# Performance work log

Measured on AMD Instinct MI355X. Metric: run time of the kernel, lower is better.

Reference implementation:

```python
import jax, jax.numpy as jnp
import numpy as np

B, M, C, IMG, P, D, L, H, DFF, NC = 16, 4, 3, 224, 16, 768, 12, 12, 3072, 1000
G = IMG // P
S = G * G + 1
HD = D // H
EPS = 1e-6
SCALE = HD ** -0.5


def setup_inputs() -> dict:
    key = jax.random.key(0)
    ks = jax.random.split(key, 12)
    w = lambda k, shape: (jax.random.normal(k, shape) * 0.02).astype(jnp.float32)
    return {
        'x': jax.random.normal(ks[0], (B, C, IMG, IMG), jnp.float32),
        'x_tangent': jax.random.normal(ks[1], (B, M, C, IMG, IMG), jnp.float32),
        'patch_w': w(ks[2], (D, C * P * P)), 'patch_b': jnp.zeros((D,), jnp.float32),
        'cls_token': w(ks[3], (1, 1, D)), 'pos_embed': w(ks[4], (1, S, D)),
        'ln1_g': jnp.ones((L, D), jnp.float32), 'ln1_b': jnp.zeros((L, D), jnp.float32),
        'qkv_w': w(ks[5], (L, 3 * D, D)), 'qkv_b': jnp.zeros((L, 3 * D), jnp.float32),
        'proj_w': w(ks[6], (L, D, D)), 'proj_b': jnp.zeros((L, D), jnp.float32),
        'ln2_g': jnp.ones((L, D), jnp.float32), 'ln2_b': jnp.zeros((L, D), jnp.float32),
        'fc1_w': w(ks[7], (L, DFF, D)), 'fc1_b': jnp.zeros((L, DFF), jnp.float32),
        'fc2_w': w(ks[8], (L, D, DFF)), 'fc2_b': jnp.zeros((L, D), jnp.float32),
        'normf_g': jnp.ones((D,), jnp.float32), 'normf_b': jnp.zeros((D,), jnp.float32),
        'head_w': w(ks[9], (NC, D)), 'head_b': jnp.zeros((NC,), jnp.float32),
    }


def _patchify(img):
    # [b,C,IMG,IMG] -> [b, G*G, C*P*P], matching Conv2d(patch) weight layout (c, ph, pw)
    b = img.shape[0]
    p = img.reshape(b, C, G, P, G, P).transpose(0, 2, 4, 1, 3, 5)
    return p.reshape(b, G * G, C * P * P)


def _ln_jvp(x, t, g, b):
    # x: [B,S,D], t: [B,M,S,D]; params constant w.r.t. tangent directions
    mu = x.mean(-1, keepdims=True)
    xc = x - mu
    inv = jax.lax.rsqrt((xc * xc).mean(-1, keepdims=True) + EPS)
    xh = xc * inv
    y = xh * g + b
    xh_b, inv_b = xh[:, None], inv[:, None]
    ty = g * inv_b * (t - t.mean(-1, keepdims=True) - xh_b * (xh_b * t).mean(-1, keepdims=True))
    return y, ty


def _gelu_jvp(x, t):
    # exact (erf) GELU and its derivative; x: [B,S,F], t: [B,M,S,F]
    cdf = 0.5 * (1.0 + jax.lax.erf(x * 0.7071067811865476))
    pdf = jnp.exp(-0.5 * x * x) * 0.3989422804014327
    return x * cdf, t * (cdf + x * pdf)[:, None]


def _softmax_jvp(s, ts):
    # s: [B,H,S,S], ts: [B,M,H,S,S]
    a = jax.nn.softmax(s, axis=-1)
    a_b = a[:, None]
    ta = a_b * (ts - (a_b * ts).sum(-1, keepdims=True))
    return a, ta


def reference(x, x_tangent, patch_w, patch_b, cls_token, pos_embed,
              ln1_g, ln1_b, qkv_w, qkv_b, proj_w, proj_b, ln2_g, ln2_b,
              fc1_w, fc1_b, fc2_w, fc2_b, normf_g, normf_b, head_w, head_b):
    # patch embed (primal + tangent; bias/pos/cls are constants -> zero tangent)
    h = _patchify(x) @ patch_w.T + patch_b                                  # [B,N,D]
    th = (_patchify(x_tangent.reshape(B * M, C, IMG, IMG)) @ patch_w.T).reshape(B, M, G * G, D)
    cls = jnp.broadcast_to(cls_token, (B, 1, D))
    h = jnp.concatenate([cls, h], axis=1) + pos_embed                       # [B,S,D]
    th = jnp.concatenate([jnp.zeros((B, M, 1, D), th.dtype), th], axis=2)   # [B,M,S,D]

    for l in range(L):
        # --- attention (manual JVP, matching the torch einsum path) ---
        y, ty = _ln_jvp(h, th, ln1_g[l], ln1_b[l])
        qkv = y @ qkv_w[l].T + qkv_b[l]
        tqkv = ty @ qkv_w[l].T
        q, k, v = jnp.split(qkv, 3, axis=-1)
        tq, tk, tv = jnp.split(tqkv, 3, axis=-1)
        q = q.reshape(B, S, H, HD); k = k.reshape(B, S, H, HD); v = v.reshape(B, S, H, HD)
        tq = tq.reshape(B, M, S, H, HD); tk = tk.reshape(B, M, S, H, HD); tv = tv.reshape(B, M, S, H, HD)
        s = jnp.einsum('bqhd,bkhd->bhqk', q, k) * SCALE
        ts = (jnp.einsum('bmqhd,bkhd->bmhqk', tq, k)
              + jnp.einsum('bqhd,bmkhd->bmhqk', q, tk)) * SCALE
        a, ta = _softmax_jvp(s, ts)
        o = jnp.einsum('bhqk,bkhd->bqhd', a, v).reshape(B, S, D)
        to = (jnp.einsum('bmhqk,bkhd->bmqhd', ta, v)
              + jnp.einsum('bhqk,bmkhd->bmqhd', a, tv)).reshape(B, M, S, D)
        h = h + o @ proj_w[l].T + proj_b[l]
        th = th + to @ proj_w[l].T
        # --- mlp ---
        y, ty = _ln_jvp(h, th, ln2_g[l], ln2_b[l])
        y = y @ fc1_w[l].T + fc1_b[l]
        ty = ty @ fc1_w[l].T
        y, ty = _gelu_jvp(y, ty)
        h = h + y @ fc2_w[l].T + fc2_b[l]
        th = th + ty @ fc2_w[l].T

    y, ty = _ln_jvp(h, th, normf_g, normf_b)
    logits = y[:, 0] @ head_w.T + head_b            # token pooling
    tlogits = ty[:, :, 0] @ head_w.T                 # [B,M,NC]
    return logits, tlogits
```

## Files before the change

kernel.cpp:

```cpp
#include <hip/hip_runtime.h>
#include <hip/hip_bf16.h>

#define DEVI __device__ __forceinline__

typedef short  bf16x8 __attribute__((ext_vector_type(8)));
typedef float  f32x4  __attribute__((ext_vector_type(4)));
typedef float  f32x4v __attribute__((ext_vector_type(4)));

static constexpr int BB   = 16;
static constexpr int MM   = 4;
static constexpr int CC   = 3;
static constexpr int IMG  = 224;
static constexpr int PPP  = 16;
static constexpr int DD   = 768;
static constexpr int LL   = 12;
static constexpr int HH   = 12;
static constexpr int DFF  = 3072;
static constexpr int NCLS = 1000;
static constexpr int GG   = 14;
static constexpr int SS   = 197;
static constexpr int HD   = 64;
static constexpr int BT   = BB*SS;
static constexpr int BMT  = BB*MM*SS;
static constexpr int RT   = BT+BMT;
static constexpr int RP   = 15872;
static constexpr int SP   = 208;
static constexpr int QLD  = 3*DD;
static constexpr int PRP  = BB*GG*GG;
static constexpr int PRT  = (BB+BB*MM)*GG*GG;
static constexpr float EPSV  = 1e-6f;
static constexpr float SCALE = 0.125f;

static constexpr int NQW  = QLD*DD;
static constexpr int NPW  = DD*DD;
static constexpr int NF1W = DFF*DD;
static constexpr int NF2W = DD*DFF;
static constexpr int WTOT = NQW+NPW+NF1W+NF2W;

DEVI unsigned short f2bf(float x){
  union { float f; unsigned u; } v; v.f = x;
  unsigned r = v.u + 0x7fffu + ((v.u>>16)&1u);
  return (unsigned short)(r>>16);
}
DEVI float bf2f(unsigned short x){
  union { unsigned u; float f; } v; v.u = ((unsigned)x)<<16;
  return v.f;
}
DEVI f32x4 mfma16(bf16x8 a, bf16x8 b, f32x4 c){
  return __builtin_amdgcn_mfma_f32_16x16x32_bf16(a,b,c,0,0,0);
}
typedef const void __attribute__((address_space(1)))* gas1;
typedef void __attribute__((address_space(3)))* las3;


DEVI bf16x8 cvt8(const float* src){
  float4 a = *(const float4*)src;
  float4 b = *(const float4*)(src+4);
  bf16x8 o;
  o[0]=(short)f2bf(a.x); o[1]=(short)f2bf(a.y); o[2]=(short)f2bf(a.z); o[3]=(short)f2bf(a.w);
  o[4]=(short)f2bf(b.x); o[5]=(short)f2bf(b.y); o[6]=(short)f2bf(b.z); o[7]=(short)f2bf(b.w);
  return o;
}

__global__ __launch_bounds__(256) void f2bf8_kernel(const float* __restrict__ in,
    unsigned short* __restrict__ out, size_t n8){
  size_t i = (size_t)blockIdx.x*256 + threadIdx.x;
  if (i < n8) *(bf16x8*)(out + i*8) = cvt8(in + i*8);
}

__global__ __launch_bounds__(256) void conv_all_v(const float* __restrict__ qkvw,
    const float* __restrict__ projw, const float* __restrict__ f1w,
    const float* __restrict__ f2w, unsigned short* __restrict__ wl){
  int l = blockIdx.y;
  size_t i = ((size_t)blockIdx.x*256 + threadIdx.x)*8;
  const float* src;
  if (i < NQW)                src = qkvw + (size_t)l*NQW + i;
  else if (i < NQW+NPW)       src = projw + (size_t)l*NPW + (i-NQW);
  else if (i < NQW+NPW+NF1W)  src = f1w + (size_t)l*NF1W + (i-NQW-NPW);
  else                        src = f2w + (size_t)l*NF2W + (i-NQW-NPW-NF1W);
  *(bf16x8*)(wl + (size_t)l*WTOT + i) = cvt8(src);
}

__global__ __launch_bounds__(256) void conv_layer_v(const float* __restrict__ qkvw,
    const float* __restrict__ projw, const float* __restrict__ f1w,
    const float* __restrict__ f2w, unsigned short* __restrict__ wl){
  size_t i = ((size_t)blockIdx.x*256 + threadIdx.x)*8;
  const float* src;
  if (i < NQW)                src = qkvw + i;
  else if (i < NQW+NPW)       src = projw + (i-NQW);
  else if (i < NQW+NPW+NF1W)  src = f1w + (i-NQW-NPW);
  else                        src = f2w + (i-NQW-NPW-NF1W);
  *(bf16x8*)(wl + i) = cvt8(src);
}

__global__ __launch_bounds__(256) void init_h(float* __restrict__ hh,
    const float* __restrict__ cls, const float* __restrict__ pos,
    const float* __restrict__ patch_b){
  size_t i = (size_t)blockIdx.x*256 + threadIdx.x;
  int r = (int)(i/DD), c = (int)(i%DD);
  float v = 0.f;
  if (r < BT){
    int s_ = r % SS;
    v = pos[(size_t)s_*DD + c] + (s_==0 ? cls[c] : patch_b[c]);
  }
  hh[i] = v;
}

__global__ __launch_bounds__(256) void patchify_k(const float* __restrict__ x,
    const float* __restrict__ xt, unsigned short* __restrict__ pat){
  size_t i = (size_t)blockIdx.x*256 + threadIdx.x;
  int r = (int)(i/DD), kk = (int)(i%DD);
  int c = kk>>8, rem = kk&255, py = rem>>4, px = rem&15;
  const float* src;
  if (r < PRP){
    int b_ = r/(GG*GG), p = r%(GG*GG);
    src = x + (((size_t)b_*CC + c)*IMG + (size_t)(p/GG)*PPP + py)*IMG + (p%GG)*PPP + px;
  } else {
    int rr = r-PRP; int bm = rr/(GG*GG), p = rr%(GG*GG);
    src = xt + (((size_t)bm*CC + c)*IMG + (size_t)(p/GG)*PPP + py)*IMG + (p%GG)*PPP + px;
  }
  pat[i] = f2bf(*src);
}


DEVI void blockSum4(float&a,float&b,float&c,float&d,float* red){
  #pragma unroll
  for (int off=32; off; off>>=1){
    a += __shfl_xor(a,off,64); b += __shfl_xor(b,off,64);
    c += __shfl_xor(c,off,64); d += __shfl_xor(d,off,64);
  }
  int w = threadIdx.x>>6;
  if ((threadIdx.x&63)==0){ red[w]=a; red[4+w]=b; red[8+w]=c; red[12+w]=d; }
  __syncthreads();
  a = red[0]+red[1]+red[2]+red[3];
  b = red[4]+red[5]+red[6]+red[7];
  c = red[8]+red[9]+red[10]+red[11];
  d = red[12]+red[13]+red[14]+red[15];
  __syncthreads();
}

__global__ __launch_bounds__(256) void ln_group(const float* __restrict__ hh,
    const float* __restrict__ g, const float* __restrict__ bb,
    unsigned short* __restrict__ ybf){
  __shared__ float red[4][10];
  int r = blockIdx.x;
  int b_ = r/SS, s_ = r%SS;
  int t = threadIdx.x;
  const float* xx = hh + (size_t)r*DD;
  float x0=xx[t], x1=xx[t+256], x2=xx[t+512];
  size_t trow[4];
  float tv[4][3];
  #pragma unroll
  for (int m=0;m<4;m++){
    trow[m] = (size_t)BT + ((size_t)(b_*MM+m))*SS + s_;
    const float* tt = hh + trow[m]*DD;
    tv[m][0]=tt[t]; tv[m][1]=tt[t+256]; tv[m][2]=tt[t+512];
  }
  float s[10];
  s[0]=x0+x1+x2; s[1]=x0*x0+x1*x1+x2*x2;
  #pragma unroll
  for (int m=0;m<4;m++){
    s[2+2*m]=tv[m][0]+tv[m][1]+tv[m][2];
    s[3+2*m]=x0*tv[m][0]+x1*tv[m][1]+x2*tv[m][2];
  }
  #pragma unroll
  for (int k=0;k<10;k++){
    float v = s[k];
    #pragma unroll
    for (int off=32; off; off>>=1) v += __shfl_xor(v, off, 64);
    s[k] = v;
  }
  int w = t>>6;
  if ((t&63)==0){
    #pragma unroll
    for (int k=0;k<10;k++) red[w][k]=s[k];
  }
  __syncthreads();
  #pragma unroll
  for (int k=0;k<10;k++) s[k] = red[0][k]+red[1][k]+red[2][k]+red[3][k];
  float mu  = s[0]*(1.f/DD);
  float inv = rsqrtf(s[1]*(1.f/DD) - mu*mu + EPSV);
  float g0=g[t], g1=g[t+256], g2=g[t+512];
  float h0=(x0-mu)*inv, h1=(x1-mu)*inv, h2=(x2-mu)*inv;
  {
    unsigned short* y = ybf + (size_t)r*DD;
    y[t]     = f2bf(h0*g0 + bb[t]);
    y[t+256] = f2bf(h1*g1 + bb[t+256]);
    y[t+512] = f2bf(h2*g2 + bb[t+512]);
  }
  #pragma unroll
  for (int m=0;m<4;m++){
    float tmean = s[2+2*m]*(1.f/DD);
    float dot   = inv*(s[3+2*m]*(1.f/DD) - mu*tmean);
    unsigned short* y = ybf + trow[m]*DD;
    y[t]     = f2bf(g0*inv*(tv[m][0] - tmean - h0*dot));
    y[t+256] = f2bf(g1*inv*(tv[m][1] - tmean - h1*dot));
    y[t+512] = f2bf(g2*inv*(tv[m][2] - tmean - h2*dot));
  }
}

__global__ __launch_bounds__(256) void ln_head(const float* __restrict__ hh,
    const float* __restrict__ g, const float* __restrict__ bb,
    unsigned short* __restrict__ ybf){
  __shared__ float red[16];
  int ri = blockIdx.x;
  int t = threadIdx.x;
  if (ri < BB){
    size_t row = (size_t)ri*SS;
    const float* x = hh + row*DD;
    float x0=x[t], x1=x[t+256], x2=x[t+512];
    float s1=x0+x1+x2, s2=x0*x0+x1*x1+x2*x2, s3=0.f, s4=0.f;
    blockSum4(s1,s2,s3,s4,red);
    float mu  = s1*(1.f/DD);
    float inv = rsqrtf(s2*(1.f/DD) - mu*mu + EPSV);
    unsigned short* y = ybf + row*DD;
    y[t]     = f2bf((x0-mu)*inv*g[t]     + bb[t]);
    y[t+256] = f2bf((x1-mu)*inv*g[t+256] + bb[t+256]);
    y[t+512] = f2bf((x2-mu)*inv*g[t+512] + bb[t+512]);
  } else {
    int t2 = ri - BB;
    size_t row = (size_t)BT + (size_t)t2*SS;
    size_t prow = (size_t)(t2/MM)*SS;
    const float* tt = hh + row*DD;
    const float* xx = hh + prow*DD;
    float t0=tt[t], t1=tt[t+256], t2v=tt[t+512];
    float x0=xx[t], x1=xx[t+256], x2=xx[t+512];
    float s1=x0+x1+x2, s2=x0*x0+x1*x1+x2*x2;
    float s3=t0+t1+t2v, s4=x0*t0+x1*t1+x2*t2v;
    blockSum4(s1,s2,s3,s4,red);
    float mu  = s1*(1.f/DD);
    float inv = rsqrtf(s2*(1.f/DD) - mu*mu + EPSV);
    float tmean = s3*(1.f/DD);
    float dot   = inv*(s4*(1.f/DD) - mu*tmean);
    unsigned short* y = ybf + row*DD;
    y[t]     = f2bf(g[t]    *inv*(t0  - tmean - (x0-mu)*inv*dot));
    y[t+256] = f2bf(g[t+256]*inv*(t1  - tmean - (x1-mu)*inv*dot));
    y[t+512] = f2bf(g[t+512]*inv*(t2v - tmean - (x2-mu)*inv*dot));
  }
}


template<int MODE>
__global__ __launch_bounds__(256,2) void gemm_bt(
    const unsigned short* __restrict__ A,
    const unsigned short* __restrict__ Aalt, int asplit, int lda,
    const unsigned short* __restrict__ W, int K, int N, int Mrows,
    float* __restrict__ outf, unsigned short* __restrict__ outb, int ldc,
    const float* __restrict__ bias, int bias_limit)
{
  __shared__ __attribute__((aligned(16))) unsigned short As[128*64];
  __shared__ __attribute__((aligned(16))) unsigned short Bs[128*64];
  const int tid = threadIdx.x;
  const int wave = tid>>6, lane = tid&63;
  const int tM = blockIdx.y, tN = blockIdx.x;
  f32x4 acc[4][4];
  f32x4 zf = {0.f,0.f,0.f,0.f};
  #pragma unroll
  for (int m=0;m<4;m++)
    #pragma unroll
    for (int n=0;n<4;n++) acc[m][n] = zf;
  const int wm = wave>>1, wn = wave&1;
  const int lrow = lane&15, lk8 = (lane>>4)<<3;
  const int srow = tid>>3;
  const int scol = (tid&7)<<3;
  const size_t arow0 = (size_t)tM*128;
  const size_t brow0 = (size_t)tN*128;

  for (int k0=0; k0<K; k0+=64){
    #pragma unroll
    for (int i=0;i<4;i++){
      int row = (int)arow0 + srow + i*32;
      const unsigned short* abase = (row < asplit) ? Aalt : A;
      const unsigned short* ga = abase + (size_t)row*lda + (k0+scol);
      __builtin_amdgcn_global_load_lds((gas1)ga, (las3)(As + i*2048 + wave*512), 16, 0, 0);
      const unsigned short* gb = W + (brow0+srow+i*32)*(size_t)K + (k0+scol);
      __builtin_amdgcn_global_load_lds((gas1)gb, (las3)(Bs + i*2048 + wave*512), 16, 0, 0);
    }
    __syncthreads();
    #pragma unroll
    for (int kk=0; kk<64; kk+=32){
      bf16x8 af[4], bw[4];
      #pragma unroll
      for (int m=0;m<4;m++) af[m] = *(const bf16x8*)(As + (wm*64+m*16+lrow)*64 + kk+lk8);
      #pragma unroll
      for (int n=0;n<4;n++) bw[n] = *(const bf16x8*)(Bs + (wn*64+n*16+lrow)*64 + kk+lk8);
      #pragma unroll
      for (int m=0;m<4;m++)
        #pragma unroll
        for (int n=0;n<4;n++)
          acc[m][n] = mfma16(af[m], bw[n], acc[m][n]);
    }
    __syncthreads();
  }

  const int colbase = tN*128 + wn*64 + lrow;
  const int rowbase = tM*128 + wm*64 + ((lane>>4)<<2);
  #pragma unroll
  for (int n=0;n<4;n++){
    int col = colbase + n*16;
    #pragma unroll
    for (int m=0;m<4;m++){
      #pragma unroll
      for (int i=0;i<4;i++){
        int r = rowbase + m*16 + i;
        float v = acc[m][n][i];
        if (MODE==0){
          if (r < bias_limit) v += bias[col];
          outb[(size_t)r*ldc + col] = f2bf(v);
        } else if (MODE==1){
          if (r < Mrows){
            if (r < bias_limit) v += bias[col];
            outf[(size_t)r*ldc + col] += v;
          }
        } else {
          if (r < PRT){
            int orow;
            if (r < PRP) orow = (r/196)*197 + 1 + r%196;
            else { int rr = r-PRP; orow = BT + (rr/196)*197 + 1 + rr%196; }
            outf[(size_t)orow*ldc + col] += v;
          }
        }
      }
    }
  }
}

__global__ __launch_bounds__(256) void transpose_v(const unsigned short* __restrict__ qkv,
    unsigned short* __restrict__ vT, unsigned short* __restrict__ tvT){
  __shared__ unsigned short tile[SP*65];
  int inst = blockIdx.x;
  size_t rowbase; unsigned short* dst; int h;
  if (inst < BB*HH){ int b_=inst/HH; h=inst%HH; rowbase=(size_t)b_*SS; dst = vT + (size_t)inst*HD*SP; }
  else { int i2=inst-BB*HH; int bm=i2/HH; h=i2%HH; rowbase=(size_t)BT+(size_t)bm*SS; dst = tvT + (size_t)i2*HD*SP; }
  int coff = 2*DD + h*HD;
  for (int i=threadIdx.x; i<SP*HD; i+=256){
    int k = i>>6, d = i&63;
    unsigned short v = (k<SS) ? qkv[(rowbase+k)*QLD + coff + d] : (unsigned short)0;
    tile[k*65+d] = v;
  }
  __syncthreads();
  for (int i=threadIdx.x; i<HD*SP; i+=256){
    int d = i/SP, k = i%SP;
    dst[(size_t)d*SP + k] = tile[k*65+d];
  }
}

__global__ __launch_bounds__(256) void attn_s1(const unsigned short* __restrict__ qkv,
                                               unsigned short* __restrict__ abf){
  int qt = blockIdx.x, inst = blockIdx.y;
  int wave = threadIdx.x>>6, lane = threadIdx.x&63;
  int lrow = lane&15, lk = (lane>>4)<<3;
  int q0 = qt*64 + wave*16;
  f32x4 acc[13];
  f32x4 zf = {0.f,0.f,0.f,0.f};
  #pragma unroll
  for (int n=0;n<13;n++) acc[n]=zf;
  int h = inst % HH, b_ = inst / HH;
  size_t prow = (size_t)b_*SS;
  const unsigned short* Ab = qkv + (prow + q0 + lrow)*QLD + h*HD + lk;
  const unsigned short* Bb = qkv + prow*QLD + DD + h*HD + lk;
  #pragma unroll
  for (int kk=0; kk<HD; kk+=32){
    bf16x8 av = *(const bf16x8*)(Ab + kk);
    #pragma unroll
    for (int n=0;n<13;n++){
      bf16x8 bv = *(const bf16x8*)(Bb + (size_t)(n*16+lrow)*QLD + kk);
      acc[n] = mfma16(av, bv, acc[n]);
    }
  }
  int grp = lane>>4;
  unsigned short* obase = abf + (size_t)inst*SP*SP;
  bool okc12 = (lrow < 5);
  #pragma unroll
  for (int i=0;i<4;i++){
    int qr = q0 + grp*4 + i;
    float val[13], e[13];
    float mv = -1e30f;
    #pragma unroll
    for (int n=0;n<13;n++){
      val[n] = acc[n][i]*SCALE;
      if (n<12 || okc12) mv = fmaxf(mv, val[n]);
    }
    #pragma unroll
    for (int off=8; off; off>>=1) mv = fmaxf(mv, __shfl_xor(mv, off, 64));
    float s = 0.f;
    #pragma unroll
    for (int n=0;n<13;n++){
      e[n] = (n<12 || okc12) ? __expf(val[n]-mv) : 0.f;
      s += e[n];
    }
    #pragma unroll
    for (int off=8; off; off>>=1) s += __shfl_xor(s, off, 64);
    float inv = 1.f/s;
    if (qr < SS){
      unsigned short* orow = obase + (size_t)qr*SP;
      #pragma unroll
      for (int n=0;n<13;n++) orow[n*16+lrow] = f2bf(e[n]*inv);
    }
  }
}

__global__ __launch_bounds__(256) void attn_s2(const unsigned short* __restrict__ qkv,
    const unsigned short* __restrict__ abf, unsigned short* __restrict__ tabf,
    int bmix0){
  int qt = blockIdx.x, il = blockIdx.y;
  int wave = threadIdx.x>>6, lane = threadIdx.x&63;
  int lrow = lane&15, lk = (lane>>4)<<3;
  int q0 = qt*64 + wave*16;
  f32x4 acc[13];
  f32x4 zf = {0.f,0.f,0.f,0.f};
  #pragma unroll
  for (int n=0;n<13;n++) acc[n]=zf;
  int h = il % HH;
  int bmix = bmix0 + il / HH;
  int b_ = bmix / MM;
  int bh = b_*HH + h;
  size_t prow = (size_t)b_*SS;
  size_t trow = (size_t)BT + (size_t)bmix*SS;
  #pragma unroll
  for (int p=0;p<2;p++){
    size_t ar = (p==0) ? trow : prow;
    size_t br = (p==1) ? trow : prow;
    const unsigned short* Ab = qkv + (ar + q0 + lrow)*QLD + h*HD + lk;
    const unsigned short* Bb = qkv + br*QLD + DD + h*HD + lk;
    #pragma unroll
    for (int kk=0; kk<HD; kk+=32){
      bf16x8 av = *(const bf16x8*)(Ab + kk);
      #pragma unroll
      for (int n=0;n<13;n++){
        bf16x8 bv = *(const bf16x8*)(Bb + (size_t)(n*16+lrow)*QLD + kk);
        acc[n] = mfma16(av, bv, acc[n]);
      }
    }
  }
  int grp = lane>>4;
  const unsigned short* abase = abf + (size_t)bh*SP*SP;
  unsigned short* tbase = tabf + (size_t)il*SP*SP;
  #pragma unroll
  for (int i=0;i<4;i++){
    int qr = q0 + grp*4 + i;
    int qc = (qr < SS) ? qr : (SS-1);
    const unsigned short* arow = abase + (size_t)qc*SP;
    float av[13], tv[13];
    float dot = 0.f;
    #pragma unroll
    for (int n=0;n<13;n++){
      tv[n] = acc[n][i]*SCALE;
      av[n] = bf2f(arow[n*16+lrow]);
      dot += av[n]*tv[n];
    }
    #pragma unroll
    for (int off=8; off; off>>=1) dot += __shfl_xor(dot, off, 64);
    if (qr < SS){
      unsigned short* trow_ = tbase + (size_t)qr*SP;
      #pragma unroll
      for (int n=0;n<13;n++) trow_[n*16+lrow] = f2bf(av[n]*(tv[n]-dot));
    }
  }
}

template<int NP>
__global__ __launch_bounds__(256) void attn_pv(
    const unsigned short* __restrict__ abf, const unsigned short* __restrict__ tabf,
    const unsigned short* __restrict__ vT,  const unsigned short* __restrict__ tvT,
    unsigned short* __restrict__ obf, int bmix0){
  int qt = blockIdx.x, il = blockIdx.y;
  int wave = threadIdx.x>>6, lane = threadIdx.x&63;
  int lrow = lane&15, lk = (lane>>4)<<3;
  int q0 = qt*64 + wave*16;
  int h = il % HH;
  int bmix = (NP==1) ? (il/HH) : (bmix0 + il/HH);
  int b_ = (NP==1) ? bmix : bmix/MM;
  int bh = b_*HH + h;
  f32x4 acc[4];
  f32x4 zf = {0.f,0.f,0.f,0.f};
  #pragma unroll
  for (int n=0;n<4;n++) acc[n]=zf;
  int arow = q0 + lrow; if (arow > SP-1) arow = SP-1;
  #pragma unroll
  for (int p=0;p<NP;p++){
    const unsigned short* Ab = (NP==2 && p==0) ? tabf + (size_t)il*SP*SP
                                               : abf + (size_t)bh*SP*SP;
    const unsigned short* Bb = (NP==2 && p==1) ? tvT + (size_t)(bmix*HH+h)*HD*SP
                                               : vT + (size_t)bh*HD*SP;
    #pragma unroll
    for (int ks=0; ks<6; ks++){
      int kb = ks*32 + lk;
      bf16x8 av = *(const bf16x8*)(Ab + (size_t)arow*SP + kb);
      #pragma unroll
      for (int n=0;n<4;n++){
        bf16x8 bv = *(const bf16x8*)(Bb + (size_t)(n*16+lrow)*SP + kb);
        acc[n] = mfma16(av, bv, acc[n]);
      }
    }
    {
      int kb = 192 + lk;
      const bf16x8 ZV = {0,0,0,0,0,0,0,0};
      bool ok = (lk < 16);
      bf16x8 av = ok ? *(const bf16x8*)(Ab + (size_t)arow*SP + kb) : ZV;
      #pragma unroll
      for (int n=0;n<4;n++){
        bf16x8 bv = ok ? *(const bf16x8*)(Bb + (size_t)(n*16+lrow)*SP + kb) : ZV;
        acc[n] = mfma16(av, bv, acc[n]);
      }
    }
  }
  size_t orow0 = (NP==1) ? (size_t)bmix*SS : (size_t)BT + (size_t)bmix*SS;
  int qr0 = q0 + ((lane>>4)<<2);
  #pragma unroll
  for (int n=0;n<4;n++){
    int cc = h*HD + n*16 + lrow;
    #pragma unroll
    for (int i=0;i<4;i++){
      int qr = qr0 + i;
      if (qr < SS) obf[(orow0+qr)*DD + cc] = f2bf(acc[n][i]);
    }
  }
}

__global__ __launch_bounds__(256) void gelu_group(unsigned short* __restrict__ fc1o,
                                                  unsigned short* __restrict__ pgbf){
  int r = blockIdx.x;
  int b_ = r/SS, s_ = r%SS;
  const bf16x8* pb = (const bf16x8*)(fc1o + (size_t)r*DFF);
  bf16x8* pg = (bf16x8*)(pgbf + (size_t)r*DFF);
  bf16x8* tb[4];
  #pragma unroll
  for (int m=0;m<4;m++)
    tb[m] = (bf16x8*)(fc1o + ((size_t)BT + (size_t)(b_*MM+m)*SS + s_)*DFF);
  for (int c = threadIdx.x; c < DFF/8; c += 256){
    bf16x8 xv = pb[c];
    float deriv[8];
    bf16x8 o;
    #pragma unroll
    for (int j=0;j<8;j++){
      float x = bf2f((unsigned short)xv[j]);
      float cdf = 0.5f*(1.f + erff(x*0.70710678118654752f));
      float pdf = __expf(-0.5f*x*x)*0.39894228040143267f;
      o[j] = (short)f2bf(x*cdf);
      deriv[j] = cdf + x*pdf;
    }
    pg[c] = o;
    #pragma unroll
    for (int m=0;m<4;m++){
      bf16x8 tv8 = tb[m][c];
      bf16x8 w;
      #pragma unroll
      for (int j=0;j<8;j++) w[j] = (short)f2bf(bf2f((unsigned short)tv8[j])*deriv[j]);
      tb[m][c] = w;
    }
  }
}

__global__ __launch_bounds__(256) void head_k(const unsigned short* __restrict__ ybf,
    const float* __restrict__ hw, const float* __restrict__ hb, float* __restrict__ out){
  __shared__ float ysh[DD];
  int ri = blockIdx.x;
  size_t yrow; float* o; bool wb;
  if (ri < BB){ yrow = (size_t)ri*SS; o = out + (size_t)ri*NCLS; wb = true; }
  else { int t2 = ri-BB; yrow = (size_t)BT + (size_t)t2*SS; o = out + (size_t)BB*NCLS + (size_t)t2*NCLS; wb = false; }
  for (int d=threadIdx.x; d<DD; d+=256) ysh[d] = bf2f(ybf[yrow*DD + d]);
  __syncthreads();
  for (int n=threadIdx.x; n<NCLS; n+=256){
    const float* wrow = hw + (size_t)n*DD;
    float acc = wb ? hb[n] : 0.f;
    for (int d=0; d<DD; d++) acc += ysh[d]*wrow[d];
    o[n] = acc;
  }
}

extern "C" void kernel_launch(void* const* d_in, const int* in_sizes, int n_in,
                              void* d_out, int out_size, void* d_ws, size_t ws_size,
                              hipStream_t stream)
{
  const float* x      = (const float*)d_in[0];
  const float* xt     = (const float*)d_in[1];
  const float* patch_w= (const float*)d_in[2];
  const float* patch_b= (const float*)d_in[3];
  const float* cls    = (const float*)d_in[4];
  const float* pos    = (const float*)d_in[5];
  const float* ln1_g  = (const float*)d_in[6];
  const float* ln1_b  = (const float*)d_in[7];
  const float* qkv_w  = (const float*)d_in[8];
  const float* qkv_b  = (const float*)d_in[9];
  const float* proj_w = (const float*)d_in[10];
  const float* proj_b = (const float*)d_in[11];
  const float* ln2_g  = (const float*)d_in[12];
  const float* ln2_b  = (const float*)d_in[13];
  const float* fc1_w  = (const float*)d_in[14];
  const float* fc1_b  = (const float*)d_in[15];
  const float* fc2_w  = (const float*)d_in[16];
  const float* fc2_b  = (const float*)d_in[17];
  const float* nf_g   = (const float*)d_in[18];
  const float* nf_b   = (const float*)d_in[19];
  const float* head_w = (const float*)d_in[20];
  const float* head_b = (const float*)d_in[21];
  float* out = (float*)d_out;

  char* ws = (char*)d_ws;
  size_t off = 0;
  auto alloc = [&](size_t bytes)->char*{
    char* p = ws + off;
    off = (off + bytes + 255) & ~(size_t)255;
    return p;
  };

  unsigned short *w_patch, *wl, *ybf, *qkvbf, *vT, *tvT, *abf, *tabf, *fc1o, *pgbf;
  float *hh;
  auto layout = [&](bool allw, int nbm)->size_t{
    off = 0;
    w_patch = (unsigned short*)alloc((size_t)DD*DD*2);
    wl      = (unsigned short*)alloc((size_t)WTOT*2*(allw?LL:1));
    hh      = (float*)alloc((size_t)RP*DD*4);
    ybf     = (unsigned short*)alloc((size_t)RP*DD*2);
    size_t slab0 = off;
    qkvbf = (unsigned short*)alloc((size_t)RP*QLD*2);
    vT    = (unsigned short*)alloc((size_t)BB*HH*HD*SP*2);
    tvT   = (unsigned short*)alloc((size_t)BB*MM*HH*HD*SP*2);
    abf   = (unsigned short*)alloc((size_t)BB*HH*SP*SP*2);
    tabf  = (unsigned short*)alloc((size_t)nbm*HH*SP*SP*2);
    size_t endA = off;
    off = slab0;
    fc1o = (unsigned short*)alloc((size_t)RP*DFF*2);
    pgbf = (unsigned short*)alloc((size_t)BT*DFF*2);
    size_t endB = off;
    return (endA > endB) ? endA : endB;
  };

  bool allw = true; int nbm = BB*MM;
  size_t need = layout(true, BB*MM);
  if (need > ws_size){ need = layout(true, BB*MM/4);  allw=true;  nbm=BB*MM/4; }
  if (need > ws_size){ need = layout(false, BB*MM);   allw=false; nbm=BB*MM;   }
  if (need > ws_size){ need = layout(false, BB*MM/4); allw=false; nbm=BB*MM/4; }
  if (need > ws_size){
    hipMemsetAsync(d_out, 0x7f, (size_t)out_size*4, stream);
    return;
  }
  int nch = (BB*MM)/nbm;

  dim3 blk(256);
  f2bf8_kernel<<<dim3((DD*DD/8+255)/256), blk, 0, stream>>>(patch_w, w_patch, (size_t)DD*DD/8);
  if (allw)
    conv_all_v<<<dim3(WTOT/8/256, LL), blk, 0, stream>>>(qkv_w, proj_w, fc1_w, fc2_w, wl);
  init_h<<<dim3((RP*DD)/256), blk, 0, stream>>>(hh, cls, pos, patch_b);
  patchify_k<<<dim3((PRT*DD)/256), blk, 0, stream>>>(x, xt, ybf);
  gemm_bt<2><<<dim3(DD/128, 123), blk, 0, stream>>>(ybf, nullptr, 0, DD, w_patch, DD, DD, PRT,
                                                    hh, nullptr, DD, nullptr, 0);

  for (int l=0; l<LL; l++){
    if (!allw)
      conv_layer_v<<<dim3(WTOT/8/256), blk, 0, stream>>>(qkv_w+(size_t)l*NQW, proj_w+(size_t)l*NPW,
                                                         fc1_w+(size_t)l*NF1W, fc2_w+(size_t)l*NF2W, wl);
    const unsigned short* w_qkv = wl + (allw ? (size_t)l*WTOT : 0);
    const unsigned short* w_proj= w_qkv + NQW;
    const unsigned short* w_fc1 = w_qkv + NQW + NPW;
    const unsigned short* w_fc2 = w_qkv + NQW + NPW + NF1W;

    ln_group<<<dim3(BT), blk, 0, stream>>>(hh, ln1_g+(size_t)l*DD, ln1_b+(size_t)l*DD, ybf);
    gemm_bt<0><<<dim3(QLD/128, RP/128), blk, 0, stream>>>(ybf, nullptr, 0, DD, w_qkv,
        DD, QLD, RT, nullptr, qkvbf, QLD, qkv_b+(size_t)l*QLD, BT);
    transpose_v<<<dim3(BB*HH + BB*MM*HH), blk, 0, stream>>>(qkvbf, vT, tvT);
    attn_s1<<<dim3(4, BB*HH), blk, 0, stream>>>(qkvbf, abf);
    attn_pv<1><<<dim3(4, BB*HH), blk, 0, stream>>>(abf, nullptr, vT, nullptr, ybf, 0);
    for (int c=0; c<nch; c++){
      attn_s2<<<dim3(4, nbm*HH), blk, 0, stream>>>(qkvbf, abf, tabf, c*nbm);
      attn_pv<2><<<dim3(4, nbm*HH), blk, 0, stream>>>(abf, tabf, vT, tvT, ybf, c*nbm);
    }
    gemm_bt<1><<<dim3(DD/128, RP/128), blk, 0, stream>>>(ybf, nullptr, 0, DD, w_proj,
        DD, DD, RT, hh, nullptr, DD, proj_b+(size_t)l*DD, BT);
    ln_group<<<dim3(BT), blk, 0, stream>>>(hh, ln2_g+(size_t)l*DD, ln2_b+(size_t)l*DD, ybf);
    gemm_bt<0><<<dim3(DFF/128, RP/128), blk, 0, stream>>>(ybf, nullptr, 0, DD, w_fc1,
        DD, DFF, RT, nullptr, fc1o, DFF, fc1_b+(size_t)l*DFF, BT);
    gelu_group<<<dim3(BT), blk, 0, stream>>>(fc1o, pgbf);
    gemm_bt<1><<<dim3(DD/128, RP/128), blk, 0, stream>>>(fc1o, pgbf, BT, DFF, w_fc2,
        DFF, DD, RT, hh, nullptr, DD, fc2_b+(size_t)l*DD, BT);
  }

  ln_head<<<dim3(BB + BB*MM), blk, 0, stream>>>(hh, nf_g, nf_b, ybf);
  head_k<<<dim3(BB + BB*MM), blk, 0, stream>>>(ybf, head_w, head_b, out);
}
```

Before: 7.969 ms.

## Fuse attention score/softmax with PV matmul via shared-memory probability tiles

Merges the softmax stage and the PV matmul into one kernel for both the primal and tangent attention paths. Probabilities and tangent probabilities are staged in LDS, so the tangent probability buffer (tabf) is no longer written to and re-read from global memory. Removing tabf also removes the chunked launch loop and its workspace fallback. The cost is 27–54 KB of LDS per block, which may lower occupancy, plus extra block-wide syncs.

```diff
diff --git a/kernel.cpp b/kernel.cpp
--- a/kernel.cpp
+++ b/kernel.cpp
@@ -5,7 +5,6 @@
 
 typedef short  bf16x8 __attribute__((ext_vector_type(8)));
 typedef float  f32x4  __attribute__((ext_vector_type(4)));
-typedef float  f32x4v __attribute__((ext_vector_type(4)));
 
 static constexpr int BB   = 16;
 static constexpr int MM   = 4;
@@ -25,6 +24,7 @@
 static constexpr int RT   = BT+BMT;
 static constexpr int RP   = 15872;
 static constexpr int SP   = 208;
+static constexpr int LDP  = 216;
 static constexpr int QLD  = 3*DD;
 static constexpr int PRP  = BB*GG*GG;
 static constexpr int PRT  = (BB+BB*MM)*GG*GG;
@@ -345,8 +345,10 @@
   }
 }
 
-__global__ __launch_bounds__(256) void attn_s1(const unsigned short* __restrict__ qkv,
-                                               unsigned short* __restrict__ abf){
+__global__ __launch_bounds__(256) void attn_s1_pv(const unsigned short* __restrict__ qkv,
+    unsigned short* __restrict__ abf, const unsigned short* __restrict__ vT,
+    unsigned short* __restrict__ obf){
+  __shared__ __attribute__((aligned(16))) unsigned short pa[64*LDP];
   int qt = blockIdx.x, inst = blockIdx.y;
   int wave = threadIdx.x>>6, lane = threadIdx.x&63;
   int lrow = lane&15, lk = (lane>>4)<<3;
@@ -392,29 +394,81 @@
     #pragma unroll
     for (int off=8; off; off>>=1) s += __shfl_xor(s, off, 64);
     float inv = 1.f/s;
-    if (qr < SS){
-      unsigned short* orow = obase + (size_t)qr*SP;
-      #pragma unroll
-      for (int n=0;n<13;n++) orow[n*16+lrow] = f2bf(e[n]*inv);
-    }
-  }
-}
-
-__global__ __launch_bounds__(256) void attn_s2(const unsigned short* __restrict__ qkv,
-    const unsigned short* __restrict__ abf, unsigned short* __restrict__ tabf,
-    int bmix0){
+    unsigned short* lrp = pa + (size_t)(wave*16 + grp*4 + i)*LDP;
+    unsigned short* orow = obase + (size_t)qr*SP;
+    #pragma unroll
+    for (int n=0;n<13;n++){
+      unsigned short pv_ = f2bf(e[n]*inv);
+      lrp[n*16+lrow] = pv_;
+      if (qr < SS) orow[n*16+lrow] = pv_;
+    }
+  }
+  __syncthreads();
+  f32x4 pacc[4];
+  #pragma unroll
+  for (int n=0;n<4;n++) pacc[n]=zf;
+  const unsigned short* Vb = vT + (size_t)inst*HD*SP;
+  const unsigned short* Arow = pa + (size_t)(wave*16 + lrow)*LDP;
+  #pragma unroll
+  for (int ks=0; ks<6; ks++){
+    int kb = ks*32 + lk;
+    bf16x8 av = *(const bf16x8*)(Arow + kb);
+    #pragma unroll
+    for (int n=0;n<4;n++){
+      bf16x8 bv = *(const bf16x8*)(Vb + (size_t)(n*16+lrow)*SP + kb);
+      pacc[n] = mfma16(av, bv, pacc[n]);
+    }
+  }
+  {
+    int kb = 192 + lk;
+    const bf16x8 ZV = {0,0,0,0,0,0,0,0};
+    bool ok = (lk < 16);
+    bf16x8 av = ok ? *(const bf16x8*)(Arow + kb) : ZV;
+    #pragma unroll
+    for (int n=0;n<4;n++){
+      bf16x8 bv = ok ? *(const bf16x8*)(Vb + (size_t)(n*16+lrow)*SP + kb) : ZV;
+      pacc[n] = mfma16(av, bv, pacc[n]);
+    }
+  }
+  size_t orow0 = (size_t)b_*SS;
+  int qr0 = q0 + (grp<<2);
+  #pragma unroll
+  for (int n=0;n<4;n++){
+    int cc = h*HD + n*16 + lrow;
+    #pragma unroll
+    for (int i=0;i<4;i++){
+      int qr = qr0 + i;
+      if (qr < SS) obf[(orow0+qr)*DD + cc] = f2bf(pacc[n][i]);
+    }
+  }
+}
+
+__global__ __launch_bounds__(256) void attn_s2_pv(const unsigned short* __restrict__ qkv,
+    const unsigned short* __restrict__ abf, const unsigned short* __restrict__ vT,
+    const unsigned short* __restrict__ tvT, unsigned short* __restrict__ obf){
+  __shared__ __attribute__((aligned(16))) unsigned short sa[64*LDP];
+  __shared__ __attribute__((aligned(16))) unsigned short ta[64*LDP];
   int qt = blockIdx.x, il = blockIdx.y;
   int wave = threadIdx.x>>6, lane = threadIdx.x&63;
   int lrow = lane&15, lk = (lane>>4)<<3;
   int q0 = qt*64 + wave*16;
+  int h = il % HH;
+  int bmix = il / HH;
+  int b_ = bmix / MM;
+  int bh = b_*HH + h;
+  {
+    const unsigned short* abase = abf + (size_t)bh*SP*SP;
+    int qb = qt*64;
+    for (int c = threadIdx.x; c < 64*26; c += 256){
+      int rl = c/26, c8 = (c%26)*8;
+      int qr = qb + rl; if (qr > SS-1) qr = SS-1;
+      *(bf16x8*)(sa + (size_t)rl*LDP + c8) = *(const bf16x8*)(abase + (size_t)qr*SP + c8);
+    }
+  }
   f32x4 acc[13];
   f32x4 zf = {0.f,0.f,0.f,0.f};
   #pragma unroll
   for (int n=0;n<13;n++) acc[n]=zf;
-  int h = il % HH;
-  int bmix = bmix0 + il / HH;
-  int b_ = bmix / MM;
-  int bh = b_*HH + h;
   size_t prow = (size_t)b_*SS;
   size_t trow = (size_t)BT + (size_t)bmix*SS;
   #pragma unroll
@@ -433,14 +487,12 @@
       }
     }
   }
+  __syncthreads();
   int grp = lane>>4;
-  const unsigned short* abase = abf + (size_t)bh*SP*SP;
-  unsigned short* tbase = tabf + (size_t)il*SP*SP;
   #pragma unroll
   for (int i=0;i<4;i++){
-    int qr = q0 + grp*4 + i;
-    int qc = (qr < SS) ? qr : (SS-1);
-    const unsigned short* arow = abase + (size_t)qc*SP;
+    int rl = wave*16 + grp*4 + i;
+    const unsigned short* arow = sa + (size_t)rl*LDP;
     float av[13], tv[13];
     float dot = 0.f;
     #pragma unroll
@@ -451,69 +503,50 @@
     }
     #pragma unroll
     for (int off=8; off; off>>=1) dot += __shfl_xor(dot, off, 64);
-    if (qr < SS){
-      unsigned short* trow_ = tbase + (size_t)qr*SP;
-      #pragma unroll
-      for (int n=0;n<13;n++) trow_[n*16+lrow] = f2bf(av[n]*(tv[n]-dot));
-    }
-  }
-}
-
-template<int NP>
-__global__ __launch_bounds__(256) void attn_pv(
-    const unsigned short* __restrict__ abf, const unsigned short* __restrict__ tabf,
-    const unsigned short* __restrict__ vT,  const unsigned short* __restrict__ tvT,
-    unsigned short* __restrict__ obf, int bmix0){
-  int qt = blockIdx.x, il = blockIdx.y;
-  int wave = threadIdx.x>>6, lane = threadIdx.x&63;
-  int lrow = lane&15, lk = (lane>>4)<<3;
-  int q0 = qt*64 + wave*16;
-  int h = il % HH;
-  int bmix = (NP==1) ? (il/HH) : (bmix0 + il/HH);
-  int b_ = (NP==1) ? bmix : bmix/MM;
-  int bh = b_*HH + h;
-  f32x4 acc[4];
-  f32x4 zf = {0.f,0.f,0.f,0.f};
-  #pragma unroll
-  for (int n=0;n<4;n++) acc[n]=zf;
-  int arow = q0 + lrow; if (arow > SP-1) arow = SP-1;
-  #pragma unroll
-  for (int p=0;p<NP;p++){
-    const unsigned short* Ab = (NP==2 && p==0) ? tabf + (size_t)il*SP*SP
-                                               : abf + (size_t)bh*SP*SP;
-    const unsigned short* Bb = (NP==2 && p==1) ? tvT + (size_t)(bmix*HH+h)*HD*SP
-                                               : vT + (size_t)bh*HD*SP;
+    unsigned short* trp = ta + (size_t)rl*LDP;
+    #pragma unroll
+    for (int n=0;n<13;n++) trp[n*16+lrow] = f2bf(av[n]*(tv[n]-dot));
+  }
+  __syncthreads();
+  f32x4 pacc[4];
+  #pragma unroll
+  for (int n=0;n<4;n++) pacc[n]=zf;
+  #pragma unroll
+  for (int p=0;p<2;p++){
+    const unsigned short* Arow = (p==0 ? ta : sa) + (size_t)(wave*16 + lrow)*LDP;
+    const unsigned short* Bb = (p==0) ? vT + (size_t)bh*HD*SP
+                                      : tvT + (size_t)il*HD*SP;
     #pragma unroll
     for (int ks=0; ks<6; ks++){
       int kb = ks*32 + lk;
-      bf16x8 av = *(const bf16x8*)(Ab + (size_t)arow*SP + kb);
+      bf16x8 av = *(const bf16x8*)(Arow + kb);
       #pragma unroll
       for (int n=0;n<4;n++){
         bf16x8 bv = *(const bf16x8*)(Bb + (size_t)(n*16+lrow)*SP + kb);
-        acc[n] = mfma16(av, bv, acc[n]);
+        pacc[n] = mfma16(av, bv, pacc[n]);
       }
     }
     {
       int kb = 192 + lk;
       const bf16x8 ZV = {0,0,0,0,0,0,0,0};
       bool ok = (lk < 16);
-      bf16x8 av = ok ? *(const bf16x8*)(Ab + (size_t)arow*SP + kb) : ZV;
+      bf16x8 av = ok ? *(const bf16x8*)(Arow + kb) : ZV;
       #pragma unroll
       for (int n=0;n<4;n++){
         bf16x8 bv = ok ? *(const bf16x8*)(Bb + (size_t)(n*16+lrow)*SP + kb) : ZV;
-        acc[n] = mfma16(av, bv, acc[n]);
+        pacc[n] = mfma16(av, bv, pacc[n]);
       }
     }
   }
-  size_t orow0 = (NP==1) ? (size_t)bmix*SS : (size_t)BT + (size_t)bmix*SS;
-  int qr0 = q0 + ((lane>>4)<<2);
+  size_t orow0 = (size_t)BT + (size_t)bmix*SS;
+  int qr0 = q0 + (grp<<2);
   #pragma unroll
   for (int n=0;n<4;n++){
     int cc = h*HD + n*16 + lrow;
     #pragma unroll
     for (int i=0;i<4;i++){
       int qr = qr0 + i;
-      if (qr < SS) obf[(orow0+qr)*DD + cc] = f2bf(acc[n][i]);
+      if (qr < SS) obf[(orow0+qr)*DD + cc] = f2bf(pacc[n][i]);
     }
   }
 }
@@ -605,9 +638,9 @@
     return p;
   };
 
-  unsigned short *w_patch, *wl, *ybf, *qkvbf, *vT, *tvT, *abf, *tabf, *fc1o, *pgbf;
+  unsigned short *w_patch, *wl, *ybf, *qkvbf, *vT, *tvT, *abf, *fc1o, *pgbf;
   float *hh;
-  auto layout = [&](bool allw, int nbm)->size_t{
+  auto layout = [&](bool allw)->size_t{
     off = 0;
     w_patch = (unsigned short*)alloc((size_t)DD*DD*2);
     wl      = (unsigned short*)alloc((size_t)WTOT*2*(allw?LL:1));
@@ -618,7 +651,6 @@
     vT    = (unsigned short*)alloc((size_t)BB*HH*HD*SP*2);
     tvT   = (unsigned short*)alloc((size_t)BB*MM*HH*HD*SP*2);
     abf   = (unsigned short*)alloc((size_t)BB*HH*SP*SP*2);
-    tabf  = (unsigned short*)alloc((size_t)nbm*HH*SP*SP*2);
     size_t endA = off;
     off = slab0;
     fc1o = (unsigned short*)alloc((size_t)RP*DFF*2);
@@ -627,16 +659,13 @@
     return (endA > endB) ? endA : endB;
   };
 
-  bool allw = true; int nbm = BB*MM;
-  size_t need = layout(true, BB*MM);
-  if (need > ws_size){ need = layout(true, BB*MM/4);  allw=true;  nbm=BB*MM/4; }
-  if (need > ws_size){ need = layout(false, BB*MM);   allw=false; nbm=BB*MM;   }
-  if (need > ws_size){ need = layout(false, BB*MM/4); allw=false; nbm=BB*MM/4; }
+  bool allw = true;
+  size_t need = layout(true);
+  if (need > ws_size){ need = layout(false); allw = false; }
   if (need > ws_size){
-    hipMemsetAsync(d_out, 0x7f, (size_t)out_size*4, stream);
+    (void)hipMemsetAsync(d_out, 0x7f, (size_t)out_size*4, stream);
     return;
   }
-  int nch = (BB*MM)/nbm;
 
   dim3 blk(256);
   f2bf8_kernel<<<dim3((DD*DD/8+255)/256), blk, 0, stream>>>(patch_w, w_patch, (size_t)DD*DD/8);
@@ -660,12 +689,8 @@
     gemm_bt<0><<<dim3(QLD/128, RP/128), blk, 0, stream>>>(ybf, nullptr, 0, DD, w_qkv,
         DD, QLD, RT, nullptr, qkvbf, QLD, qkv_b+(size_t)l*QLD, BT);
     transpose_v<<<dim3(BB*HH + BB*MM*HH), blk, 0, stream>>>(qkvbf, vT, tvT);
-    attn_s1<<<dim3(4, BB*HH), blk, 0, stream>>>(qkvbf, abf);
-    attn_pv<1><<<dim3(4, BB*HH), blk, 0, stream>>>(abf, nullptr, vT, nullptr, ybf, 0);
-    for (int c=0; c<nch; c++){
-      attn_s2<<<dim3(4, nbm*HH), blk, 0, stream>>>(qkvbf, abf, tabf, c*nbm);
-      attn_pv<2><<<dim3(4, nbm*HH), blk, 0, stream>>>(abf, tabf, vT, tvT, ybf, c*nbm);
-    }
+    attn_s1_pv<<<dim3(4, BB*HH), blk, 0, stream>>>(qkvbf, abf, vT, ybf);
+    attn_s2_pv<<<dim3(4, BB*MM*HH), blk, 0, stream>>>(qkvbf, abf, vT, tvT, ybf);
     gemm_bt<1><<<dim3(DD/128, RP/128), blk, 0, stream>>>(ybf, nullptr, 0, DD, w_proj,
         DD, DD, RT, hh, nullptr, DD, proj_b+(size_t)l*DD, BT);
     ln_group<<<dim3(BT), blk, 0, stream>>>(hh, ln2_g+(size_t)l*DD, ln2_b+(size_t)l*DD, ybf);
```

Measured after the change: 7.476 ms (median of 2 runs). 6.2% less time.
